# Performance work log

Hardware: AMD Instinct MI355X
Metric: run time of the kernel (lower is better)

## Reference

```python
import jax, jax.numpy as jnp
import numpy as np

B, C, H, W = 4, 128, 64, 64
CI = C // 2  # inter_channels
BN_EPS = 1e-5


def _conv1x1(x, w, b):
    # x: [B,C,H,W], w: [O,C], b: [O] -> [B,O,H,W]
    return jnp.einsum('bchw,oc->bohw', x, w) + b[None, :, None, None]


def setup_inputs() -> dict:
    key = jax.random.key(0)
    ks = jax.random.split(key, 11)
    s_in = 1.0 / np.sqrt(C)
    s_mid = 1.0 / np.sqrt(CI)
    return {
        'x': jax.random.normal(ks[0], (B, C, H, W), dtype=jnp.float32),
        'g_w': jax.random.normal(ks[1], (CI, C), dtype=jnp.float32) * s_in,
        'g_b': jax.random.normal(ks[2], (CI,), dtype=jnp.float32) * 0.01,
        'theta_w': jax.random.normal(ks[3], (CI, C), dtype=jnp.float32) * s_in,
        'theta_b': jax.random.normal(ks[4], (CI,), dtype=jnp.float32) * 0.01,
        'phi_w': jax.random.normal(ks[5], (CI, C), dtype=jnp.float32) * s_in,
        'phi_b': jax.random.normal(ks[6], (CI,), dtype=jnp.float32) * 0.01,
        'w_w': jax.random.normal(ks[7], (C, CI), dtype=jnp.float32) * s_mid,
        'w_b': jax.random.normal(ks[8], (C,), dtype=jnp.float32) * 0.01,
        'bn_gamma': jnp.ones((C,), dtype=jnp.float32),
        'bn_beta': jnp.zeros((C,), dtype=jnp.float32),
    }


def reference(x, g_w, g_b, theta_w, theta_b, phi_w, phi_b, w_w, w_b, bn_gamma, bn_beta):
    b, c, h, w = x.shape
    n = h * w
    # 1x1 conv projections, flattened over spatial positions -> [B,N,CI]
    g_x = _conv1x1(x, g_w, g_b).reshape(b, CI, n).transpose(0, 2, 1)
    theta_x = _conv1x1(x, theta_w, theta_b).reshape(b, CI, n).transpose(0, 2, 1)
    phi_x = _conv1x1(x, phi_w, phi_b).reshape(b, CI, n)  # [B,CI,N]
    # full attention over spatial tokens: [B,N,N]
    f = jnp.einsum('bnc,bcm->bnm', theta_x, phi_x)
    f_div_c = jax.nn.softmax(f, axis=-1)
    y = jnp.einsum('bnm,bmc->bnc', f_div_c, g_x)  # [B,N,CI]
    y = y.transpose(0, 2, 1).reshape(b, CI, h, w)
    w_y = _conv1x1(y, w_w, w_b)  # [B,C,H,W]
    # BatchNorm2d (training-mode batch statistics over B,H,W)
    mean = jnp.mean(w_y, axis=(0, 2, 3))
    var = jnp.var(w_y, axis=(0, 2, 3))
    bn = bn_gamma[None, :, None, None] * (w_y - mean[None, :, None, None]) \
         * jax.lax.rsqrt(var + BN_EPS)[None, :, None, None] + bn_beta[None, :, None, None]
    return bn + x
```

## Files before the change

### kernel.cpp

```cpp
#include <hip/hip_runtime.h>
#include <hip/hip_bf16.h>
#include <math.h>

#define NSP 4096
#define CC  128
#define CIC 64
#define NB  4
#define LOG2E 1.4426950408889634f

typedef unsigned short u16;
typedef unsigned int u32;
typedef short s8bf __attribute__((ext_vector_type(8)));
typedef float f32x4 __attribute__((ext_vector_type(4)));
typedef float f32x2 __attribute__((ext_vector_type(2)));
typedef float f32x16 __attribute__((ext_vector_type(16)));

#define MFMA32(a, b, c) __builtin_amdgcn_mfma_f32_32x32x16_bf16(a, b, c, 0, 0, 0)

#define WSB_PB    0
#define WSB_TH    (NB * CIC * NSP * 2)
#define WSB_PH    (WSB_TH + NB * NSP * CIC * 2)
#define WSB_OP    (WSB_PH + NB * NSP * CIC * 2)
#define WSB_LP    (WSB_OP + (size_t)NB * 2 * NSP * CIC * 4)
#define WSB_WT4   (WSB_LP + NB * 2 * NSP * 4)
#define WSB_WT2P  (WSB_WT4 + CC * 256 * 4)
#define WSB_P2    (WSB_WT2P + CIC * CC * 4)

__device__ __forceinline__ u16 f2bf(float f) {
    union { float f; unsigned u; } v; v.f = f;
    unsigned r = v.u + 0x7fffu + ((v.u >> 16) & 1u);
    return (u16)(r >> 16);
}

__global__ __launch_bounds__(256) void prep_kernel(
    const float* __restrict__ g_w, const float* __restrict__ t_w,
    const float* __restrict__ p_w, const float* __restrict__ w_w,
    float* __restrict__ wT4, float* __restrict__ wT2p)
{
    const int c = blockIdx.x;
    const int o = threadIdx.x;
    if (o < 192) {
        float v;
        if (o < 64)       v = g_w[o * CC + c];
        else if (o < 128) v = t_w[(o - 64) * CC + c] * LOG2E;
        else              v = p_w[(o - 128) * CC + c];
        wT4[(c << 8) + ((o & 63) << 2) + (o >> 6)] = v;
    } else {
        wT4[(c << 8) + ((o - 192) << 2) + 3] = 0.f;
    }
    if (o < CIC)
        wT2p[(o << 7) + ((c & 63) << 1) + (c >> 6)] = w_w[c * CIC + o];
}

__global__ __launch_bounds__(512) void proj_kernel(
    const float* __restrict__ x, const float* __restrict__ wT4,
    const float* __restrict__ g_b, const float* __restrict__ t_b,
    const float* __restrict__ p_b,
    u16* __restrict__ PB, u16* __restrict__ th_tm, u16* __restrict__ ph_tm)
{
    __shared__ float Xs[CC][68];
    __shared__ u16 Ot[192][72];

    const int b    = blockIdx.y;
    const int n0   = blockIdx.x * 64;
    const int tid  = threadIdx.x;
    const int lane = tid & 63;
    const int wv   = tid >> 6;
    const int t0   = wv * 8;

    const float* xb = x + (size_t)b * CC * NSP + n0;
    #pragma unroll
    for (int k = 0; k < 4; ++k) {
        int idx = tid + (k << 9);
        int c = idx >> 4, t4 = (idx & 15) << 2;
        *(f32x4*)&Xs[c][t4] = *(const f32x4*)(xb + (size_t)c * NSP + t4);
    }
    __syncthreads();

    float acc[3][8];
    {
        float b0 = g_b[lane], b1 = t_b[lane] * LOG2E, b2 = p_b[lane];
        #pragma unroll
        for (int t = 0; t < 8; ++t) { acc[0][t] = b0; acc[1][t] = b1; acc[2][t] = b2; }
    }

    const float* wp = wT4 + (lane << 2);
    #pragma unroll 4
    for (int c = 0; c < CC; ++c) {
        f32x4 wv4 = *(const f32x4*)(wp + (c << 8));
        f32x4 xv0 = *(const f32x4*)&Xs[c][t0];
        f32x4 xv1 = *(const f32x4*)&Xs[c][t0 + 4];
        #pragma unroll
        for (int t = 0; t < 4; ++t) {
            acc[0][t]     += wv4[0] * xv0[t];
            acc[0][4 + t] += wv4[0] * xv1[t];
            acc[1][t]     += wv4[1] * xv0[t];
            acc[1][4 + t] += wv4[1] * xv1[t];
            acc[2][t]     += wv4[2] * xv0[t];
            acc[2][4 + t] += wv4[2] * xv1[t];
        }
    }

    #pragma unroll
    for (int p = 0; p < 3; ++p) {
        #pragma unroll
        for (int i = 0; i < 4; ++i) {
            unsigned pk = (unsigned)f2bf(acc[p][2 * i]) | ((unsigned)f2bf(acc[p][2 * i + 1]) << 16);
            *(unsigned*)&Ot[lane + 64 * p][t0 + 2 * i] = pk;
        }
    }
    __syncthreads();

    {
        int row = tid >> 3, ch = tid & 7;
        uint4 v = *(const uint4*)&Ot[row][ch * 8];
        *(uint4*)(PB + (size_t)b * CIC * NSP + (size_t)row * NSP + n0 + ch * 8) = v;
    }
    #pragma unroll
    for (int k = 0; k < 2; ++k) {
        int idx = tid + (k << 9);
        int tok = idx >> 4, sel = (idx >> 3) & 1, c8 = (idx & 7) * 8;
        u16* dst = (sel ? ph_tm : th_tm) + ((size_t)b * NSP + n0 + tok) * 64 + c8;
        union { u16 t[8]; uint4 v4; } u;
        #pragma unroll
        for (int j = 0; j < 8; ++j) u.t[j] = Ot[64 + sel * 64 + c8 + j][tok];
        *(uint4*)dst = u.v4;
    }
}

__global__ __launch_bounds__(512, 2) void attn_kernel(
    const u16* __restrict__ PB, const u16* __restrict__ th_tm,
    const u16* __restrict__ ph_tm,
    float* __restrict__ O_part, float* __restrict__ l_part)
{
    const int b    = blockIdx.z;
    const int kvs  = blockIdx.y;
    const int q0   = blockIdx.x << 7;
    const int tid  = threadIdx.x;
    const int lane = tid & 63;
    const int w    = tid >> 6;
    const int s    = w & 3;
    const int h    = w >> 2;
    const int l31  = lane & 31;
    const int l5   = lane >> 5;

    __shared__ __align__(16) char KV[2][2][2][8192];

    const u16* gp = PB + (size_t)b * CIC * NSP;
    const u16* th = th_tm + (size_t)b * NSP * 64;
    const u16* ph = ph_tm + (size_t)b * NSP * 64;

    const int kb0 = kvs << 11;

    const int srow = (w << 3) + (lane >> 3);
    const int gch  = ((lane & 7) ^ (srow & 7)) << 3;
    char* dK0 = &KV[0][0][0][0] + (w << 10);
    const int woff = w << 10;

    auto stage = [&](int buf, int t) {
        const int m0 = kb0 + (t << 6);
        const u16* sK0 = ph + ((size_t)(m0 + srow) << 6) + gch;
        const u16* sK1 = ph + ((size_t)(m0 + 1024 + srow) << 6) + gch;
        const u16* sV0 = gp + (size_t)srow * NSP + m0 + gch;
        const u16* sV1 = gp + (size_t)srow * NSP + m0 + 1024 + gch;
        __builtin_amdgcn_global_load_lds(
            (const __attribute__((address_space(1))) void*)sK0,
            (__attribute__((address_space(3))) void*)(&KV[buf][0][0][0] + woff), 16, 0, 0);
        __builtin_amdgcn_global_load_lds(
            (const __attribute__((address_space(1))) void*)sK1,
            (__attribute__((address_space(3))) void*)(&KV[buf][0][1][0] + woff), 16, 0, 0);
        __builtin_amdgcn_global_load_lds(
            (const __attribute__((address_space(1))) void*)sV0,
            (__attribute__((address_space(3))) void*)(&KV[buf][1][0][0] + woff), 16, 0, 0);
        __builtin_amdgcn_global_load_lds(
            (const __attribute__((address_space(1))) void*)sV1,
            (__attribute__((address_space(3))) void*)(&KV[buf][1][1][0] + woff), 16, 0, 0);
    };
    (void)dK0;

    s8bf qb[4];
    const int qtok = q0 + (s << 5) + l31;
    #pragma unroll
    for (int fc = 0; fc < 4; ++fc)
        qb[fc] = *(const s8bf*)(th + ((size_t)qtok << 6) + fc * 16 + l5 * 8);

    f32x16 Ov0, Ov1, cinit;
    #pragma unroll
    for (int i = 0; i < 16; ++i) { Ov0[i] = 0.f; Ov1[i] = 0.f; cinit[i] = -32.f; }
    float lr = 0.f;

    stage(0, 0);
    __syncthreads();

    u32 pk[2][4][2];

    for (int t = 0; t < 16; ++t) {
        const int buf = t & 1;

        if (t < 15) stage(buf ^ 1, t + 1);

        const char* Kb = &KV[buf][0][h][0];
        const char* Vb = &KV[buf][1][h][0];

        #pragma unroll
        for (int kt = 0; kt < 2; ++kt) {
            const int trow = l31 + (kt << 5);
            const int rswz = trow & 7;
            f32x16 sv = cinit;
            __builtin_amdgcn_s_setprio(1);
            #pragma unroll
            for (int fc = 0; fc < 4; ++fc) {
                s8bf ka = *(const s8bf*)(Kb + trow * 128 + (((2 * fc + l5) ^ rswz) << 4));
                sv = MFMA32(ka, qb[fc], sv);
            }
            __builtin_amdgcn_s_setprio(0);
            float e[16];
            #pragma unroll
            for (int i = 0; i < 16; ++i) e[i] = __builtin_amdgcn_exp2f(sv[i]);
            #pragma unroll
            for (int i = 0; i < 16; ++i) lr += e[i];
            #pragma unroll
            for (int m = 0; m < 4; ++m) {
                #pragma unroll
                for (int i = 0; i < 2; ++i) {
                    __hip_bfloat162 hh = __float22bfloat162_rn(
                        make_float2(e[4 * m + 2 * i], e[4 * m + 2 * i + 1]));
                    union { __hip_bfloat162 h2; u32 u; } cv; cv.h2 = hh;
                    pk[kt][m][i] = cv.u;
                }
            }
        }

        __builtin_amdgcn_s_setprio(1);
        #pragma unroll
        for (int f = 0; f < 4; ++f) {
            const int tt = f >> 1;
            const int m0c = 2 * (f & 1);
            u32 sA0 = pk[tt][m0c][0],     sA1 = pk[tt][m0c][1];
            u32 sB0 = pk[tt][m0c + 1][0], sB1 = pk[tt][m0c + 1][1];
            u32 self0 = l5 ? sB0 : sA0, self1 = l5 ? sB1 : sA1;
            u32 send0 = l5 ? sA0 : sB0, send1 = l5 ? sA1 : sB1;
            u32 x0 = (u32)__shfl_xor((int)send0, 32);
            u32 x1 = (u32)__shfl_xor((int)send1, 32);
            union { u32 u[4]; s8bf v; } pa;
            pa.u[0] = l5 ? x0 : self0;
            pa.u[1] = l5 ? x1 : self1;
            pa.u[2] = l5 ? self0 : x0;
            pa.u[3] = l5 ? self1 : x1;
            const int c1 = l31 + 32;
            s8bf v0 = *(const s8bf*)(Vb + l31 * 128 + (((2 * f + l5) ^ (l31 & 7)) << 4));
            s8bf v1 = *(const s8bf*)(Vb + c1 * 128 + (((2 * f + l5) ^ (c1 & 7)) << 4));
            Ov0 = MFMA32(pa.v, v0, Ov0);
            Ov1 = MFMA32(pa.v, v1, Ov1);
        }
        __builtin_amdgcn_s_setprio(0);

        __syncthreads();
    }

    float lrh = lr + __shfl_xor(lr, 32);
    float* Olds = (float*)&KV[0][0][0][0];
    float* Llds = (float*)&KV[1][0][0][0];

    if (h == 1) {
        #pragma unroll
        for (int reg = 0; reg < 16; ++reg) {
            int q = (reg & 3) + 8 * (reg >> 2) + 4 * l5;
            Olds[((s << 5) + q) * 64 + l31]      = Ov0[reg];
            Olds[((s << 5) + q) * 64 + 32 + l31] = Ov1[reg];
        }
        if (l5 == 0) Llds[(s << 5) + l31] = lrh;
    }
    __syncthreads();
    if (h == 0) {
        float ltot = lrh + Llds[(s << 5) + l31];
        float* Ob = O_part + ((size_t)b * 2 + kvs) * NSP * 64;
        #pragma unroll
        for (int reg = 0; reg < 16; ++reg) {
            int q = (reg & 3) + 8 * (reg >> 2) + 4 * l5;
            int qg = q0 + (s << 5) + q;
            Ob[(size_t)qg * 64 + l31]      = Ov0[reg] + Olds[((s << 5) + q) * 64 + l31];
            Ob[(size_t)qg * 64 + 32 + l31] = Ov1[reg] + Olds[((s << 5) + q) * 64 + 32 + l31];
        }
        if (l5 == 0)
            l_part[((size_t)b * 2 + kvs) * NSP + q0 + (s << 5) + l31] = ltot;
    }
}

__global__ __launch_bounds__(256) void wconv_kernel(
    const float* __restrict__ O_part, const float* __restrict__ l_part,
    const float* __restrict__ wT2p, const float* __restrict__ w_b,
    float* __restrict__ out, float* __restrict__ parts2)
{
    __shared__ float Ys[CIC][36];
    __shared__ float Of[CC][36];

    const int b    = blockIdx.y;
    const int n0   = blockIdx.x * 32;
    const int tid  = threadIdx.x;
    const int lane = tid & 63;
    const int wv   = tid >> 6;
    const int t0   = wv * 8;

    #pragma unroll
    for (int rnd = 0; rnd < 2; ++rnd) {
        int tok = (tid >> 4) + (rnd << 4);
        int ci4 = tid & 15;
        int qg  = n0 + tok;
        f32x4 a = {0.f, 0.f, 0.f, 0.f};
        float ls = 0.f;
        #pragma unroll
        for (int kvs = 0; kvs < 2; ++kvs) {
            a += *(const f32x4*)(O_part + (((size_t)b * 2 + kvs) * NSP + qg) * 64 + (ci4 << 2));
            ls += l_part[((size_t)b * 2 + kvs) * NSP + qg];
        }
        float inv = 1.0f / ls;
        #pragma unroll
        for (int j = 0; j < 4; ++j) Ys[(ci4 << 2) + j][tok] = a[j] * inv;
    }
    __syncthreads();

    float acc[2][8];
    #pragma unroll
    for (int t = 0; t < 8; ++t) { acc[0][t] = 0.f; acc[1][t] = 0.f; }

    const float* wp = wT2p + (lane << 1);
    #pragma unroll 8
    for (int ci = 0; ci < CIC; ++ci) {
        f32x2 wv2 = *(const f32x2*)(wp + (ci << 7));
        f32x4 y0 = *(const f32x4*)&Ys[ci][t0];
        f32x4 y1 = *(const f32x4*)&Ys[ci][t0 + 4];
        #pragma unroll
        for (int t = 0; t < 4; ++t) {
            acc[0][t]     += wv2[0] * y0[t];
            acc[0][4 + t] += wv2[0] * y1[t];
            acc[1][t]     += wv2[1] * y0[t];
            acc[1][4 + t] += wv2[1] * y1[t];
        }
    }

    float b0 = w_b[lane], b1 = w_b[64 + lane];
    #pragma unroll
    for (int t = 0; t < 4; ++t) {
        Of[lane][t0 + t]          = acc[0][t] + b0;
        Of[lane][t0 + 4 + t]      = acc[0][4 + t] + b0;
        Of[64 + lane][t0 + t]     = acc[1][t] + b1;
        Of[64 + lane][t0 + 4 + t] = acc[1][4 + t] + b1;
    }
    __syncthreads();

    float* ob = out + (size_t)b * CC * NSP + n0;
    #pragma unroll
    for (int k = 0; k < 4; ++k) {
        int idx = tid + (k << 8);
        int row = idx >> 3, ch = idx & 7;
        *(float4*)(ob + (size_t)row * NSP + ch * 4) = *(const float4*)&Of[row][ch * 4];
    }

    if (tid < CC) {
        float s = 0.f, ss = 0.f;
        #pragma unroll 8
        for (int t2 = 0; t2 < 32; ++t2) {
            float v = Of[tid][t2];
            s += v; ss += v * v;
        }
        const int blk = b * (NSP / 32) + blockIdx.x;
        parts2[(size_t)tid * 1024 + blk]       = s;
        parts2[(size_t)tid * 1024 + 512 + blk] = ss;
    }
}

__global__ __launch_bounds__(256) void bn_kernel(
    const float* __restrict__ x, const float* __restrict__ parts2,
    const float* __restrict__ gamma, const float* __restrict__ beta,
    float* __restrict__ out)
{
    __shared__ float red[8];
    const int tid = threadIdx.x;
    const int i   = blockIdx.x * 256 + tid;
    const int c   = (i >> 10) & (CC - 1);

    const float* P = parts2 + (size_t)c * 1024;
    float s  = P[tid]       + P[256 + tid];
    float ss = P[512 + tid] + P[768 + tid];
    #pragma unroll
    for (int off = 32; off > 0; off >>= 1) {
        s  += __shfl_down(s, off, 64);
        ss += __shfl_down(ss, off, 64);
    }
    const int wid = tid >> 6, lane = tid & 63;
    if (lane == 0) { red[wid] = s; red[4 + wid] = ss; }
    __syncthreads();
    float st  = red[0] + red[1] + red[2] + red[3];
    float sst = red[4] + red[5] + red[6] + red[7];

    float mean = st * (1.0f / 16384.0f);
    float var  = sst * (1.0f / 16384.0f) - mean * mean;
    float istd = rsqrtf(var + 1e-5f);
    float ga = gamma[c] * istd;
    float be = beta[c] - mean * ga;
    float4 wy = ((const float4*)out)[i];
    float4 xv = ((const float4*)x)[i];
    float4 o;
    o.x = wy.x * ga + be + xv.x;
    o.y = wy.y * ga + be + xv.y;
    o.z = wy.z * ga + be + xv.z;
    o.w = wy.w * ga + be + xv.w;
    ((float4*)out)[i] = o;
}

extern "C" void kernel_launch(void* const* d_in, const int* in_sizes, int n_in,
                              void* d_out, int out_size, void* d_ws, size_t ws_size,
                              hipStream_t stream)
{
    const float* x    = (const float*)d_in[0];
    const float* g_w  = (const float*)d_in[1];
    const float* g_b  = (const float*)d_in[2];
    const float* t_w  = (const float*)d_in[3];
    const float* t_b  = (const float*)d_in[4];
    const float* p_w  = (const float*)d_in[5];
    const float* p_b  = (const float*)d_in[6];
    const float* w_w  = (const float*)d_in[7];
    const float* w_b  = (const float*)d_in[8];
    const float* bn_g = (const float*)d_in[9];
    const float* bn_b = (const float*)d_in[10];
    float* out = (float*)d_out;
    char* ws8  = (char*)d_ws;

    u16*   PB     = (u16*)(ws8 + WSB_PB);
    u16*   TH     = (u16*)(ws8 + WSB_TH);
    u16*   PH     = (u16*)(ws8 + WSB_PH);
    float* OP     = (float*)(ws8 + WSB_OP);
    float* LP     = (float*)(ws8 + WSB_LP);
    float* wT4    = (float*)(ws8 + WSB_WT4);
    float* wT2p   = (float*)(ws8 + WSB_WT2P);
    float* parts2 = (float*)(ws8 + WSB_P2);

    prep_kernel <<<dim3(CC), 256, 0, stream>>>(g_w, t_w, p_w, w_w, wT4, wT2p);
    proj_kernel <<<dim3(NSP / 64, NB), 512, 0, stream>>>(x, wT4, g_b, t_b, p_b, PB, TH, PH);
    attn_kernel <<<dim3(NSP / 128, 2, NB), 512, 0, stream>>>(PB, TH, PH, OP, LP);
    wconv_kernel<<<dim3(NSP / 32, NB), 256, 0, stream>>>(OP, LP, wT2p, w_b, out, parts2);
    bn_kernel   <<<dim3(2048), 256, 0, stream>>>(x, parts2, bn_g, bn_b, out);
}
```

Before: 69.53 us.

## Split KV four ways inside one attention block instead of across blocks

The attention kernel drops its two-way KV split across blocks. Each block now covers 64 queries and the full 4096 keys, divided among four wave groups that each take a quarter. The partial outputs and softmax sums are combined in LDS, normalized in the block, and written as a single y tensor. This removes the O_part/l_part round trip through global memory and the merge step in wconv. In exchange the block's LDS footprint doubles to 128KB, which likely limits occupancy to one block per CU, and the grid size stays the same.

```diff
diff --git a/kernel.cpp b/kernel.cpp
--- a/kernel.cpp
+++ b/kernel.cpp
@@ -20,9 +20,8 @@
 #define WSB_PB    0
 #define WSB_TH    (NB * CIC * NSP * 2)
 #define WSB_PH    (WSB_TH + NB * NSP * CIC * 2)
-#define WSB_OP    (WSB_PH + NB * NSP * CIC * 2)
-#define WSB_LP    (WSB_OP + (size_t)NB * 2 * NSP * CIC * 4)
-#define WSB_WT4   (WSB_LP + NB * 2 * NSP * 4)
+#define WSB_Y     (WSB_PH + NB * NSP * CIC * 2)
+#define WSB_WT4   (WSB_Y + (size_t)NB * NSP * CIC * 4)
 #define WSB_WT2P  (WSB_WT4 + CC * 256 * 4)
 #define WSB_P2    (WSB_WT2P + CIC * CC * 4)
 
@@ -130,53 +129,41 @@
 
 __global__ __launch_bounds__(512, 2) void attn_kernel(
     const u16* __restrict__ PB, const u16* __restrict__ th_tm,
-    const u16* __restrict__ ph_tm,
-    float* __restrict__ O_part, float* __restrict__ l_part)
+    const u16* __restrict__ ph_tm, float* __restrict__ y)
 {
     const int b    = blockIdx.z;
-    const int kvs  = blockIdx.y;
-    const int q0   = blockIdx.x << 7;
+    const int q0   = blockIdx.x << 6;
     const int tid  = threadIdx.x;
     const int lane = tid & 63;
     const int w    = tid >> 6;
-    const int s    = w & 3;
-    const int h    = w >> 2;
+    const int s    = w & 1;
+    const int h    = w >> 1;
     const int l31  = lane & 31;
     const int l5   = lane >> 5;
 
-    __shared__ __align__(16) char KV[2][2][2][8192];
+    __shared__ __align__(16) char KV[2][2][4][8192];
 
     const u16* gp = PB + (size_t)b * CIC * NSP;
     const u16* th = th_tm + (size_t)b * NSP * 64;
     const u16* ph = ph_tm + (size_t)b * NSP * 64;
 
-    const int kb0 = kvs << 11;
-
     const int srow = (w << 3) + (lane >> 3);
     const int gch  = ((lane & 7) ^ (srow & 7)) << 3;
-    char* dK0 = &KV[0][0][0][0] + (w << 10);
     const int woff = w << 10;
 
     auto stage = [&](int buf, int t) {
-        const int m0 = kb0 + (t << 6);
-        const u16* sK0 = ph + ((size_t)(m0 + srow) << 6) + gch;
-        const u16* sK1 = ph + ((size_t)(m0 + 1024 + srow) << 6) + gch;
-        const u16* sV0 = gp + (size_t)srow * NSP + m0 + gch;
-        const u16* sV1 = gp + (size_t)srow * NSP + m0 + 1024 + gch;
-        __builtin_amdgcn_global_load_lds(
-            (const __attribute__((address_space(1))) void*)sK0,
-            (__attribute__((address_space(3))) void*)(&KV[buf][0][0][0] + woff), 16, 0, 0);
-        __builtin_amdgcn_global_load_lds(
-            (const __attribute__((address_space(1))) void*)sK1,
-            (__attribute__((address_space(3))) void*)(&KV[buf][0][1][0] + woff), 16, 0, 0);
-        __builtin_amdgcn_global_load_lds(
-            (const __attribute__((address_space(1))) void*)sV0,
-            (__attribute__((address_space(3))) void*)(&KV[buf][1][0][0] + woff), 16, 0, 0);
-        __builtin_amdgcn_global_load_lds(
-            (const __attribute__((address_space(1))) void*)sV1,
-            (__attribute__((address_space(3))) void*)(&KV[buf][1][1][0] + woff), 16, 0, 0);
+        const int t64 = t << 6;
+        #pragma unroll
+        for (int qd = 0; qd < 4; ++qd) {
+            const int m0 = (qd << 10) + t64;
+            __builtin_amdgcn_global_load_lds(
+                (const __attribute__((address_space(1))) void*)(ph + ((size_t)(m0 + srow) << 6) + gch),
+                (__attribute__((address_space(3))) void*)(&KV[buf][0][qd][0] + woff), 16, 0, 0);
+            __builtin_amdgcn_global_load_lds(
+                (const __attribute__((address_space(1))) void*)(gp + (size_t)srow * NSP + m0 + gch),
+                (__attribute__((address_space(3))) void*)(&KV[buf][1][qd][0] + woff), 16, 0, 0);
+        }
     };
-    (void)dK0;
 
     s8bf qb[4];
     const int qtok = q0 + (s << 5) + l31;
@@ -196,7 +183,6 @@
 
     for (int t = 0; t < 16; ++t) {
         const int buf = t & 1;
-
         if (t < 15) stage(buf ^ 1, t + 1);
 
         const char* Kb = &KV[buf][0][h][0];
@@ -261,36 +247,56 @@
     float lrh = lr + __shfl_xor(lr, 32);
     float* Olds = (float*)&KV[0][0][0][0];
     float* Llds = (float*)&KV[1][0][0][0];
-
-    if (h == 1) {
+    float* Linv = (float*)&KV[1][1][0][0];
+
+    if (h > 0) {
         #pragma unroll
         for (int reg = 0; reg < 16; ++reg) {
             int q = (reg & 3) + 8 * (reg >> 2) + 4 * l5;
-            Olds[((s << 5) + q) * 64 + l31]      = Ov0[reg];
-            Olds[((s << 5) + q) * 64 + 32 + l31] = Ov1[reg];
-        }
-        if (l5 == 0) Llds[(s << 5) + l31] = lrh;
+            int row = (s << 5) + q;
+            Olds[((h - 1) * 64 + row) * 64 + l31]      = Ov0[reg];
+            Olds[((h - 1) * 64 + row) * 64 + 32 + l31] = Ov1[reg];
+        }
+        if (l5 == 0) Llds[(h - 1) * 64 + (s << 5) + l31] = lrh;
     }
     __syncthreads();
     if (h == 0) {
-        float ltot = lrh + Llds[(s << 5) + l31];
-        float* Ob = O_part + ((size_t)b * 2 + kvs) * NSP * 64;
+        float ltot = lrh + Llds[(s << 5) + l31] + Llds[64 + (s << 5) + l31]
+                   + Llds[128 + (s << 5) + l31];
+        if (l5 == 0) Linv[(s << 5) + l31] = 1.0f / ltot;
+    }
+    __syncthreads();
+    if (h == 0) {
         #pragma unroll
         for (int reg = 0; reg < 16; ++reg) {
             int q = (reg & 3) + 8 * (reg >> 2) + 4 * l5;
-            int qg = q0 + (s << 5) + q;
-            Ob[(size_t)qg * 64 + l31]      = Ov0[reg] + Olds[((s << 5) + q) * 64 + l31];
-            Ob[(size_t)qg * 64 + 32 + l31] = Ov1[reg] + Olds[((s << 5) + q) * 64 + 32 + l31];
-        }
-        if (l5 == 0)
-            l_part[((size_t)b * 2 + kvs) * NSP + q0 + (s << 5) + l31] = ltot;
+            int row = (s << 5) + q;
+            float inv = Linv[row];
+            float a0 = Ov0[reg] + Olds[(row)*64 + l31] + Olds[(64 + row) * 64 + l31]
+                     + Olds[(128 + row) * 64 + l31];
+            float a1 = Ov1[reg] + Olds[(row)*64 + 32 + l31] + Olds[(64 + row) * 64 + 32 + l31]
+                     + Olds[(128 + row) * 64 + 32 + l31];
+            Olds[(row)*64 + l31]      = a0 * inv;
+            Olds[(row)*64 + 32 + l31] = a1 * inv;
+        }
+    }
+    __syncthreads();
+
+    {
+        float* yb = y + ((size_t)b * NSP + q0) * 64;
+        #pragma unroll
+        for (int k = 0; k < 2; ++k) {
+            int idx = tid + (k << 9);
+            int row = idx >> 4, c4 = (idx & 15) << 2;
+            *(float4*)(yb + (size_t)row * 64 + c4) = *(const float4*)&Olds[row * 64 + c4];
+        }
     }
 }
 
 __global__ __launch_bounds__(256) void wconv_kernel(
-    const float* __restrict__ O_part, const float* __restrict__ l_part,
-    const float* __restrict__ wT2p, const float* __restrict__ w_b,
-    float* __restrict__ out, float* __restrict__ parts2)
+    const float* __restrict__ y, const float* __restrict__ wT2p,
+    const float* __restrict__ w_b, float* __restrict__ out,
+    float* __restrict__ parts2)
 {
     __shared__ float Ys[CIC][36];
     __shared__ float Of[CC][36];
@@ -306,17 +312,9 @@
     for (int rnd = 0; rnd < 2; ++rnd) {
         int tok = (tid >> 4) + (rnd << 4);
         int ci4 = tid & 15;
-        int qg  = n0 + tok;
-        f32x4 a = {0.f, 0.f, 0.f, 0.f};
-        float ls = 0.f;
-        #pragma unroll
-        for (int kvs = 0; kvs < 2; ++kvs) {
-            a += *(const f32x4*)(O_part + (((size_t)b * 2 + kvs) * NSP + qg) * 64 + (ci4 << 2));
-            ls += l_part[((size_t)b * 2 + kvs) * NSP + qg];
-        }
-        float inv = 1.0f / ls;
-        #pragma unroll
-        for (int j = 0; j < 4; ++j) Ys[(ci4 << 2) + j][tok] = a[j] * inv;
+        f32x4 a = *(const f32x4*)(y + (((size_t)b * NSP + n0 + tok) << 6) + (ci4 << 2));
+        #pragma unroll
+        for (int j = 0; j < 4; ++j) Ys[(ci4 << 2) + j][tok] = a[j];
     }
     __syncthreads();
 
@@ -430,15 +428,14 @@
     u16*   PB     = (u16*)(ws8 + WSB_PB);
     u16*   TH     = (u16*)(ws8 + WSB_TH);
     u16*   PH     = (u16*)(ws8 + WSB_PH);
-    float* OP     = (float*)(ws8 + WSB_OP);
-    float* LP     = (float*)(ws8 + WSB_LP);
+    float* Y      = (float*)(ws8 + WSB_Y);
     float* wT4    = (float*)(ws8 + WSB_WT4);
     float* wT2p   = (float*)(ws8 + WSB_WT2P);
     float* parts2 = (float*)(ws8 + WSB_P2);
 
     prep_kernel <<<dim3(CC), 256, 0, stream>>>(g_w, t_w, p_w, w_w, wT4, wT2p);
     proj_kernel <<<dim3(NSP / 64, NB), 512, 0, stream>>>(x, wT4, g_b, t_b, p_b, PB, TH, PH);
-    attn_kernel <<<dim3(NSP / 128, 2, NB), 512, 0, stream>>>(PB, TH, PH, OP, LP);
-    wconv_kernel<<<dim3(NSP / 32, NB), 256, 0, stream>>>(OP, LP, wT2p, w_b, out, parts2);
+    attn_kernel <<<dim3(NSP / 64, 1, NB), 512, 0, stream>>>(PB, TH, PH, Y);
+    wconv_kernel<<<dim3(NSP / 32, NB), 256, 0, stream>>>(Y, wT2p, w_b, out, parts2);
     bn_kernel   <<<dim3(2048), 256, 0, stream>>>(x, parts2, bn_g, bn_b, out);
 }
```

Result: slower. 72.69 us (+4.5%).
